# Optimization experiments

Hardware: AMD Instinct MI355X
Metric: run time of the kernel (lower is better)

## Reference

```python
import jax, jax.numpy as jnp
import numpy as np

H = 128
P, L, C = 1024, 1024, 128
NT, NH, NA, NB, NPA, NPE = 64, 32, 64, 64, 32, 32


def _ln(x, g, b):
    m = jnp.mean(x, -1, keepdims=True)
    v = jnp.var(x, -1, keepdims=True)
    return (x - m) * jax.lax.rsqrt(v + 1e-5) * g + b


def _lrl(x, W, b, g, be):
    # Linear -> ReLU -> LayerNorm (the Sequential block used everywhere)
    return _ln(jax.nn.relu(x @ W.T + b), g, be)


def _combine(middle, margin, rel):
    # margin-middle-margin combine: aggregate related margin geos on both sides
    # rel: (M, G) 0/1 float; middle (M,h); margin (G,h)
    agg = rel @ margin                      # (M, h)
    comb = agg + middle + agg
    mask = (jnp.sum(rel, -1) >= 2.0).astype(middle.dtype)  # need two margins
    return comb, mask


def _score(sym, geo, mask, W1, b1, g, be, W2, b2):
    # pairwise sym x geo -> Linear/ReLU/LN -> Linear(h,1), masked, sigmoid
    pair = sym[:, None, :] + geo[None, :, :]          # (N, R, h)
    hdn = _lrl(pair, W1, b1, g, be)
    logits = hdn @ W2 + b2                            # (N, R)
    return jax.nn.sigmoid(jnp.where(mask[None, :] > 0, logits, -1e9))


def setup_inputs() -> dict:
    key = jax.random.key(0)
    ks = jax.random.split(key, 16)
    s = 0.02
    inp = {
        'points': jax.random.normal(ks[0], (P, H), jnp.float32),
        'lines': jax.random.normal(ks[1], (L, H), jnp.float32),
        'circles': jax.random.normal(ks[2], (C, H), jnp.float32),
        'text_symbols': jax.random.normal(ks[3], (NT, H), jnp.float32),
        'head_symbols': jax.random.normal(ks[4], (NH, H), jnp.float32),
        'angle_symbols': jax.random.normal(ks[5], (NA, H), jnp.float32),
        'bar_symbols': jax.random.normal(ks[6], (NB, H), jnp.float32),
        'parallel_symbols': jax.random.normal(ks[7], (NPA, H), jnp.float32),
        'perpendicular_symbols': jax.random.normal(ks[8], (NPE, H), jnp.float32),
        'rel_W': jax.random.normal(ks[9], (3, H, H), jnp.float32) * s,
        'rel_b': jnp.zeros((3, H), jnp.float32),
        'rel_g': jnp.ones((3, H), jnp.float32),
        'rel_be': jnp.zeros((3, H), jnp.float32),
        'gm_W': jax.random.normal(ks[10], (2, H, H), jnp.float32) * s,
        'gm_b': jnp.zeros((2, H), jnp.float32),
        'gm_g': jnp.ones((2, H), jnp.float32),
        'gm_be': jnp.zeros((2, H), jnp.float32),
        'sc_W1': jax.random.normal(ks[11], (6, H, H), jnp.float32) * s,
        'sc_b1': jnp.zeros((6, H), jnp.float32),
        'sc_g': jnp.ones((6, H), jnp.float32),
        'sc_be': jnp.zeros((6, H), jnp.float32),
        'sc_W2': jax.random.normal(ks[12], (6, H), jnp.float32) * s,
        'sc_b2': jnp.zeros((6,), jnp.float32),
        'pl_rels': jax.random.randint(ks[13], (P, L), 0, 2, jnp.int32),
        'pc_rels': jax.random.randint(ks[14], (P, C), 0, 2, jnp.int32),
    }
    return inp


def reference(points, lines, circles, text_symbols, head_symbols,
              angle_symbols, bar_symbols, parallel_symbols, perpendicular_symbols,
              rel_W, rel_b, rel_g, rel_be, gm_W, gm_b, gm_g, gm_be,
              sc_W1, sc_b1, sc_g, sc_be, sc_W2, sc_b2, pl_rels, pc_rels):
    pl = pl_rels.astype(points.dtype)            # (P, L)
    pc = pc_rels.astype(points.dtype)            # (P, C)

    # LPL: middle=points, margin=lines, rel=pl_rels
    lpl_c, lpl_m = _combine(points, lines, pl)
    LPL = _lrl(lpl_c, rel_W[0], rel_b[0], rel_g[0], rel_be[0])   # (P, h)
    # PLP: middle=lines, margin=points, rel=pl_rels.T
    plp_c, plp_m = _combine(lines, points, pl.T)
    PLP = _lrl(plp_c, rel_W[1], rel_b[1], rel_g[1], rel_be[1])   # (L, h)
    # PCP: middle=circles, margin=points, rel=pc_rels.T
    pcp_c, pcp_m = _combine(circles, points, pc.T)
    PCP = _lrl(pcp_c, rel_W[2], rel_b[2], rel_g[2], rel_be[2])   # (C, h)

    ones = lambda n: jnp.ones((n,), points.dtype)

    def gm(x):
        x = _lrl(x, gm_W[0], gm_b[0], gm_g[0], gm_be[0])
        return _lrl(x, gm_W[1], gm_b[1], gm_g[1], gm_be[1])

    # text symbols vs (P, L, LPL, PLP, PCP, head)
    geo_t = jnp.concatenate([points, lines, LPL, PLP, PCP, head_symbols], 0)
    mask_t = jnp.concatenate([ones(P), ones(L), lpl_m, plp_m, pcp_m, ones(NH)], 0)
    text = _score(text_symbols, gm(geo_t), mask_t,
                  sc_W1[0], sc_b1[0], sc_g[0], sc_be[0], sc_W2[0], sc_b2[0])

    # head symbols vs (P, LPL, PLP, PCP)
    geo_h = jnp.concatenate([points, LPL, PLP, PCP], 0)
    mask_h = jnp.concatenate([ones(P), lpl_m, plp_m, pcp_m], 0)
    head = _score(head_symbols, gm(geo_h), mask_h,
                  sc_W1[1], sc_b1[1], sc_g[1], sc_be[1], sc_W2[1], sc_b2[1])

    angle = _score(angle_symbols, LPL, lpl_m,
                   sc_W1[2], sc_b1[2], sc_g[2], sc_be[2], sc_W2[2], sc_b2[2])
    bar = _score(bar_symbols, PLP, plp_m,
                 sc_W1[3], sc_b1[3], sc_g[3], sc_be[3], sc_W2[3], sc_b2[3])
    para = _score(parallel_symbols, lines, ones(L),
                  sc_W1[4], sc_b1[4], sc_g[4], sc_be[4], sc_W2[4], sc_b2[4])
    perp = _score(perpendicular_symbols, LPL, lpl_m,
                  sc_W1[5], sc_b1[5], sc_g[5], sc_be[5], sc_W2[5], sc_b2[5])

    return jnp.concatenate([text.ravel(), head.ravel(), angle.ravel(),
                            bar.ravel(), para.ravel(), perp.ravel()])
```

## Files before the change

kernel.cpp:

```cpp
#include <hip/hip_runtime.h>

#define HH 128

constexpr int OFF_AGGPL = 0;
constexpr int OFF_AGGLP = OFF_AGGPL + 1024*HH;
constexpr int OFF_AGGCP = OFF_AGGLP + 1024*HH;
constexpr int OFF_MLPL  = OFF_AGGCP + 128*HH;
constexpr int OFF_MPLP  = OFF_MLPL + 1024;
constexpr int OFF_MPCP  = OFF_MPLP + 1024;
constexpr int OFF_LPL   = OFF_MPCP + 128;
constexpr int OFF_PLP   = OFF_LPL + 1024*HH;
constexpr int OFF_PCP   = OFF_PLP + 1024*HH;
constexpr int OFF_G1    = OFF_PCP + 128*HH;
constexpr int OFF_GT    = OFF_G1 + 4256*HH;
constexpr int OFF_BTEXT = OFF_GT + 4256*HH;
constexpr int OFF_BHEAD = OFF_BTEXT + 4256*HH;
constexpr int OFF_BANG  = OFF_BHEAD + 3200*HH;
constexpr int OFF_BBAR  = OFF_BANG + 1024*HH;
constexpr int OFF_BPARA = OFF_BBAR + 1024*HH;
constexpr int OFF_BPERP = OFF_BPARA + 1024*HH;
constexpr int OFF_A     = OFF_BPERP + 1024*HH;
constexpr int WS_FLOATS = OFF_A + 288*HH;

__global__ __launch_bounds__(512) void k_agg(
    const int* __restrict__ pl, const int* __restrict__ pc,
    const float* __restrict__ points, const float* __restrict__ lines,
    float* __restrict__ ws)
{
    __shared__ __attribute__((aligned(16))) float smem[16384];
    float (*rel)[1024] = (float(*)[1024])smem;
    float* red = smem;
    const int t = threadIdx.x;
    const int b = blockIdx.x;
    const int hq  = t & 31;
    const int grp = t >> 5;

    const float* V; float* OUT; float* MASK; int base;
    if (b < 128) {
        base = b*8; V = lines; OUT = ws + OFF_AGGPL; MASK = ws + OFF_MLPL;
        const int4* pl4 = (const int4*)pl;
        #pragma unroll
        for (int i = 0; i < 4; ++i) {
            int idx = i*512 + t; int r = idx >> 8, lq = idx & 255;
            int4 v = pl4[(base + r)*256 + lq];
            float4 f; f.x=(float)v.x; f.y=(float)v.y; f.z=(float)v.z; f.w=(float)v.w;
            *(float4*)&rel[r][lq*4] = f;
        }
    } else if (b < 256) {
        base = (b-128)*8; V = points; OUT = ws + OFF_AGGLP; MASK = ws + OFF_MPLP;
        #pragma unroll
        for (int i = 0; i < 16; ++i) {
            int idx = i*512 + t; int c = idx & 7, k = idx >> 3;
            rel[c][k] = (float)pl[k*1024 + base + c];
        }
    } else {
        base = (b-256)*8; V = points; OUT = ws + OFF_AGGCP; MASK = ws + OFF_MPCP;
        #pragma unroll
        for (int i = 0; i < 16; ++i) {
            int idx = i*512 + t; int c = idx & 7, k = idx >> 3;
            rel[c][k] = (float)pc[k*128 + base + c];
        }
    }
    __syncthreads();
    {
        int r = t >> 6, lane = t & 63;
        float s = 0.f;
        #pragma unroll
        for (int i = 0; i < 16; ++i) s += rel[r][lane*16 + i];
        #pragma unroll
        for (int off = 32; off; off >>= 1) s += __shfl_xor(s, off, 64);
        if (lane == 0) MASK[base + r] = (s >= 2.0f) ? 1.0f : 0.0f;
    }

    float4 acc[8];
    #pragma unroll
    for (int r = 0; r < 8; ++r) acc[r] = {0.f, 0.f, 0.f, 0.f};
    const float4* V4 = (const float4*)V;
    const int l0 = grp * 64;
    #pragma unroll 4
    for (int l = l0; l < l0 + 64; l += 4) {
        float4 v0 = V4[(l+0)*32 + hq];
        float4 v1 = V4[(l+1)*32 + hq];
        float4 v2 = V4[(l+2)*32 + hq];
        float4 v3 = V4[(l+3)*32 + hq];
        #pragma unroll
        for (int r = 0; r < 8; ++r) {
            float4 rv = *(const float4*)&rel[r][l];
            acc[r].x += rv.x*v0.x + rv.y*v1.x + rv.z*v2.x + rv.w*v3.x;
            acc[r].y += rv.x*v0.y + rv.y*v1.y + rv.z*v2.y + rv.w*v3.y;
            acc[r].z += rv.x*v0.z + rv.y*v1.z + rv.z*v2.z + rv.w*v3.z;
            acc[r].w += rv.x*v0.w + rv.y*v1.w + rv.z*v2.w + rv.w*v3.w;
        }
    }
    __syncthreads();
    #pragma unroll
    for (int r = 0; r < 8; ++r)
        *(float4*)&red[(grp*8 + r)*128 + hq*4] = acc[r];
    __syncthreads();
    #pragma unroll
    for (int o = t; o < 1024; o += 512) {
        int r = o >> 7, c = o & 127;
        float s = 0.f;
        #pragma unroll
        for (int g2 = 0; g2 < 16; ++g2) s += red[g2*1024 + r*128 + c];
        OUT[(base + r)*HH + c] = s;
    }
}

__global__ __launch_bounds__(256) void k_lrl(
    int mode, float* __restrict__ ws,
    const float* __restrict__ points, const float* __restrict__ lines,
    const float* __restrict__ circles, const float* __restrict__ text_s,
    const float* __restrict__ head_s, const float* __restrict__ angle_s,
    const float* __restrict__ bar_s, const float* __restrict__ para_s,
    const float* __restrict__ perp_s,
    const float* __restrict__ rel_W, const float* __restrict__ rel_b,
    const float* __restrict__ rel_g, const float* __restrict__ rel_be,
    const float* __restrict__ gm_W, const float* __restrict__ gm_b,
    const float* __restrict__ gm_g, const float* __restrict__ gm_be,
    const float* __restrict__ sc_W1, const float* __restrict__ sc_b1)
{
    __shared__ __attribute__((aligned(16))) float Xs[32][132];
    __shared__ __attribute__((aligned(16))) float Ws[64][132];
    const int t = threadIdx.x;
    const int row0 = blockIdx.x * 32;

    const float* W = nullptr; const float* bias = nullptr;
    const float* gv = nullptr; const float* bev = nullptr;
    const float* xsrc = nullptr; const float* asrc = nullptr; const float* msrc = nullptr;
    float* outp = nullptr;
    bool do_ln = false;

    if (mode == 0) {
        do_ln = true;
        if (row0 < 1024) {
            asrc = ws + OFF_AGGPL + row0*HH; msrc = points + row0*HH;
            W = rel_W;          bias = rel_b;       gv = rel_g;       bev = rel_be;
            outp = ws + OFF_LPL + row0*HH;
        } else if (row0 < 2048) {
            int r = row0 - 1024;
            asrc = ws + OFF_AGGLP + r*HH; msrc = lines + r*HH;
            W = rel_W + 16384;  bias = rel_b + 128; gv = rel_g + 128; bev = rel_be + 128;
            outp = ws + OFF_PLP + r*HH;
        } else {
            int r = row0 - 2048;
            asrc = ws + OFF_AGGCP + r*HH; msrc = circles + r*HH;
            W = rel_W + 32768;  bias = rel_b + 256; gv = rel_g + 256; bev = rel_be + 256;
            outp = ws + OFF_PCP + r*HH;
        }
    } else if (mode == 1) {
        do_ln = true; W = gm_W; bias = gm_b; gv = gm_g; bev = gm_be;
        outp = ws + OFF_G1 + row0*HH;
        if      (row0 < 1024) xsrc = points + row0*HH;
        else if (row0 < 2048) xsrc = lines + (row0-1024)*HH;
        else if (row0 < 3072) xsrc = ws + OFF_LPL + (row0-2048)*HH;
        else if (row0 < 4096) xsrc = ws + OFF_PLP + (row0-3072)*HH;
        else if (row0 < 4224) xsrc = ws + OFF_PCP + (row0-4096)*HH;
        else                  xsrc = head_s + (row0-4224)*HH;
    } else if (mode == 2) {
        do_ln = true; W = gm_W + 16384; bias = gm_b + 128; gv = gm_g + 128; bev = gm_be + 128;
        xsrc = ws + OFF_G1 + row0*HH;
        outp = ws + OFF_GT + row0*HH;
    } else {
        do_ln = false;
        if (row0 < 4256) {
            xsrc = ws + OFF_GT + row0*HH; W = sc_W1; outp = ws + OFF_BTEXT + row0*HH;
        } else if (row0 < 7456) {
            int i0 = row0 - 4256;
            W = sc_W1 + 16384; outp = ws + OFF_BHEAD + i0*HH;
            int gtrow;
            if      (i0 < 1024) gtrow = i0;
            else if (i0 < 2048) gtrow = 2048 + (i0 - 1024);
            else if (i0 < 3072) gtrow = 3072 + (i0 - 2048);
            else                gtrow = 4096 + (i0 - 3072);
            xsrc = ws + OFF_GT + gtrow*HH;
        } else if (row0 < 8480) {
            int i0 = row0 - 7456;
            xsrc = ws + OFF_LPL + i0*HH; W = sc_W1 + 2*16384; outp = ws + OFF_BANG + i0*HH;
        } else if (row0 < 9504) {
            int i0 = row0 - 8480;
            xsrc = ws + OFF_PLP + i0*HH; W = sc_W1 + 3*16384; outp = ws + OFF_BBAR + i0*HH;
        } else if (row0 < 10528) {
            int i0 = row0 - 9504;
            xsrc = lines + i0*HH;        W = sc_W1 + 4*16384; outp = ws + OFF_BPARA + i0*HH;
        } else if (row0 < 11552) {
            int i0 = row0 - 10528;
            xsrc = ws + OFF_LPL + i0*HH; W = sc_W1 + 5*16384; outp = ws + OFF_BPERP + i0*HH;
        } else {
            int i0 = row0 - 11552;
            outp = ws + OFF_A + i0*HH;
            int k; const float* s;
            if      (i0 < 64)  { k=0; s = text_s  + i0*HH; }
            else if (i0 < 96)  { k=1; s = head_s  + (i0-64)*HH; }
            else if (i0 < 160) { k=2; s = angle_s + (i0-96)*HH; }
            else if (i0 < 224) { k=3; s = bar_s   + (i0-160)*HH; }
            else if (i0 < 256) { k=4; s = para_s  + (i0-224)*HH; }
            else               { k=5; s = perp_s  + (i0-256)*HH; }
            xsrc = s; W = sc_W1 + k*16384; bias = sc_b1 + k*128;
        }
    }

    if (asrc != nullptr) {
        #pragma unroll
        for (int i = 0; i < 4; ++i) {
            int idx = i*256 + t; int r = idx >> 5, hq = idx & 31;
            float4 a = *(const float4*)&asrc[r*HH + hq*4];
            float4 m = *(const float4*)&msrc[r*HH + hq*4];
            float4 v; v.x = 2.f*a.x+m.x; v.y = 2.f*a.y+m.y; v.z = 2.f*a.z+m.z; v.w = 2.f*a.w+m.w;
            *(float4*)&Xs[r][hq*4] = v;
        }
    } else {
        #pragma unroll
        for (int i = 0; i < 4; ++i) {
            int idx = i*256 + t; int r = idx >> 5, hq = idx & 31;
            *(float4*)&Xs[r][hq*4] = *(const float4*)&xsrc[r*HH + hq*4];
        }
    }

    const int jq = t & 31;
    const int rq = t >> 5;
    float acc[4][4] = {};
    for (int p = 0; p < 2; ++p) {
        __syncthreads();
        #pragma unroll
        for (int i = 0; i < 8; ++i) {
            int idx = i*256 + t; int j = idx >> 4, hq = idx & 15;
            float4 v = *(const float4*)&W[j*HH + p*64 + hq*4];
            Ws[hq*4+0][j] = v.x; Ws[hq*4+1][j] = v.y; Ws[hq*4+2][j] = v.z; Ws[hq*4+3][j] = v.w;
        }
        __syncthreads();
        #pragma unroll
        for (int hh = 0; hh < 64; hh += 4) {
            const int h = p*64 + hh;
            float4 x0 = *(const float4*)&Xs[rq*4+0][h];
            float4 x1 = *(const float4*)&Xs[rq*4+1][h];
            float4 x2 = *(const float4*)&Xs[rq*4+2][h];
            float4 x3 = *(const float4*)&Xs[rq*4+3][h];
            float4 w0 = *(const float4*)&Ws[hh+0][jq*4];
            float4 w1 = *(const float4*)&Ws[hh+1][jq*4];
            float4 w2 = *(const float4*)&Ws[hh+2][jq*4];
            float4 w3 = *(const float4*)&Ws[hh+3][jq*4];
            #define ROWUPD(ri, xv) \
                acc[ri][0] += xv.x*w0.x + xv.y*w1.x + xv.z*w2.x + xv.w*w3.x; \
                acc[ri][1] += xv.x*w0.y + xv.y*w1.y + xv.z*w2.y + xv.w*w3.y; \
                acc[ri][2] += xv.x*w0.z + xv.y*w1.z + xv.z*w2.z + xv.w*w3.z; \
                acc[ri][3] += xv.x*w0.w + xv.y*w1.w + xv.z*w2.w + xv.w*w3.w;
            ROWUPD(0, x0) ROWUPD(1, x1) ROWUPD(2, x2) ROWUPD(3, x3)
            #undef ROWUPD
        }
    }

    float4 bv = {0.f,0.f,0.f,0.f};
    if (bias != nullptr) bv = *(const float4*)&bias[jq*4];
    if (do_ln) {
        float4 gg = *(const float4*)&gv[jq*4];
        float4 bb = *(const float4*)&bev[jq*4];
        #pragma unroll
        for (int ri = 0; ri < 4; ++ri) {
            float y0 = fmaxf(acc[ri][0] + bv.x, 0.f);
            float y1 = fmaxf(acc[ri][1] + bv.y, 0.f);
            float y2 = fmaxf(acc[ri][2] + bv.z, 0.f);
            float y3 = fmaxf(acc[ri][3] + bv.w, 0.f);
            float s1 = y0+y1+y2+y3;
            float s2 = y0*y0+y1*y1+y2*y2+y3*y3;
            #pragma unroll
            for (int off = 16; off; off >>= 1) {
                s1 += __shfl_xor(s1, off, 32);
                s2 += __shfl_xor(s2, off, 32);
            }
            float m   = s1 * (1.0f/128.0f);
            float var = s2 * (1.0f/128.0f) - m*m;
            float sc  = rsqrtf(var + 1e-5f);
            float4 o;
            o.x = (y0 - m)*sc*gg.x + bb.x;
            o.y = (y1 - m)*sc*gg.y + bb.y;
            o.z = (y2 - m)*sc*gg.z + bb.z;
            o.w = (y3 - m)*sc*gg.w + bb.w;
            *(float4*)&outp[(rq*4+ri)*HH + jq*4] = o;
        }
    } else {
        #pragma unroll
        for (int ri = 0; ri < 4; ++ri) {
            float4 o;
            o.x = acc[ri][0] + bv.x; o.y = acc[ri][1] + bv.y;
            o.z = acc[ri][2] + bv.z; o.w = acc[ri][3] + bv.w;
            *(float4*)&outp[(rq*4+ri)*HH + jq*4] = o;
        }
    }
}

__global__ __launch_bounds__(256) void k_score(
    const float* __restrict__ ws,
    const float* __restrict__ sc_g, const float* __restrict__ sc_be,
    const float* __restrict__ sc_W2, const float* __restrict__ sc_b2,
    float* __restrict__ out)
{
    __shared__ __attribute__((aligned(16))) float As[16][132];
    __shared__ __attribute__((aligned(16))) float Bs[16][132];
    __shared__ __attribute__((aligned(16))) float gw2s[128];
    __shared__ float msk[16];
    __shared__ float red2[4];
    const int t = threadIdx.x, b = blockIdx.x;
    int k, tn, tr, Rk, Abase, outbase;
    const float* Bk;
    if (b < 1064)      { k=0; int lc=b;      tn=lc/266; tr=lc%266; Rk=4256; Abase=0;   outbase=0;      Bk = ws+OFF_BTEXT; }
    else if (b < 1464) { k=1; int lc=b-1064; tn=lc/200; tr=lc%200; Rk=3200; Abase=64;  outbase=272384; Bk = ws+OFF_BHEAD; }
    else if (b < 1720) { k=2; int lc=b-1464; tn=lc>>6;  tr=lc&63;  Rk=1024; Abase=96;  outbase=374784; Bk = ws+OFF_BANG; }
    else if (b < 1976) { k=3; int lc=b-1720; tn=lc>>6;  tr=lc&63;  Rk=1024; Abase=160; outbase=440320; Bk = ws+OFF_BBAR; }
    else if (b < 2104) { k=4; int lc=b-1976; tn=lc>>6;  tr=lc&63;  Rk=1024; Abase=224; outbase=505856; Bk = ws+OFF_BPARA; }
    else               { k=5; int lc=b-2104; tn=lc>>6;  tr=lc&63;  Rk=1024; Abase=256; outbase=538624; Bk = ws+OFF_BPERP; }

    if (t < 128) {
        float g = sc_g[k*128+t], w2 = sc_W2[k*128+t], be = sc_be[k*128+t];
        float gw = g*w2, bw = be*w2;
        gw2s[t] = gw;
        #pragma unroll
        for (int off = 32; off; off >>= 1) {
            gw += __shfl_xor(gw, off, 64);
            bw += __shfl_xor(bw, off, 64);
        }
        if ((t & 63) == 0) { red2[(t>>6)*2+0] = gw; red2[(t>>6)*2+1] = bw; }
    }
    const float* Ap = ws + OFF_A + (Abase + tn*16)*HH;
    const float* Bp = Bk + tr*16*HH;
    #pragma unroll
    for (int i = 0; i < 2; ++i) {
        int idx = i*256 + t; int r = idx >> 5, hq = idx & 31;
        *(float4*)&As[r][hq*4] = *(const float4*)&Ap[r*HH + hq*4];
        *(float4*)&Bs[r][hq*4] = *(const float4*)&Bp[r*HH + hq*4];
    }
    if (t < 16) {
        int r = tr*16 + t;
        float mv = 1.0f;
        const float* mL = ws + OFF_MLPL;
        const float* mP = ws + OFF_MPLP;
        const float* mC = ws + OFF_MPCP;
        if (k == 0) {
            if      (r >= 2048 && r < 3072) mv = mL[r-2048];
            else if (r >= 3072 && r < 4096) mv = mP[r-3072];
            else if (r >= 4096 && r < 4224) mv = mC[r-4096];
        } else if (k == 1) {
            if      (r >= 1024 && r < 2048) mv = mL[r-1024];
            else if (r >= 2048 && r < 3072) mv = mP[r-2048];
            else if (r >= 3072)             mv = mC[r-3072];
        } else if (k == 2 || k == 5) mv = mL[r];
        else if (k == 3)             mv = mP[r];
        msk[t] = mv;
    }
    __syncthreads();
    const float sgw2 = red2[0] + red2[2];
    const float cb   = red2[1] + red2[3] + sc_b2[k];
    const int ni = t >> 4, ri = t & 15;
    float s1 = 0.f, s2 = 0.f, sw = 0.f;
    #pragma unroll
    for (int h = 0; h < 128; h += 4) {
        float4 av = *(const float4*)&As[ni][h];
        float4 bv = *(const float4*)&Bs[ri][h];
        float4 wv = *(const float4*)&gw2s[h];
        float y;
        y = fmaxf(av.x + bv.x, 0.f); s1 += y; s2 += y*y; sw += y*wv.x;
        y = fmaxf(av.y + bv.y, 0.f); s1 += y; s2 += y*y; sw += y*wv.y;
        y = fmaxf(av.z + bv.z, 0.f); s1 += y; s2 += y*y; sw += y*wv.z;
        y = fmaxf(av.w + bv.w, 0.f); s1 += y; s2 += y*y; sw += y*wv.w;
    }
    float m   = s1 * (1.0f/128.0f);
    float var = s2 * (1.0f/128.0f) - m*m;
    float logit = (sw - m*sgw2) * rsqrtf(var + 1e-5f) + cb;
    float o = (msk[ri] > 0.f) ? (1.0f/(1.0f + __expf(-logit))) : 0.0f;
    out[outbase + (tn*16+ni)*Rk + tr*16 + ri] = o;
}

extern "C" void kernel_launch(void* const* d_in, const int* in_sizes, int n_in,
                              void* d_out, int out_size, void* d_ws, size_t ws_size,
                              hipStream_t stream)
{
    const float* points  = (const float*)d_in[0];
    const float* lines   = (const float*)d_in[1];
    const float* circles = (const float*)d_in[2];
    const float* text_s  = (const float*)d_in[3];
    const float* head_s  = (const float*)d_in[4];
    const float* angle_s = (const float*)d_in[5];
    const float* bar_s   = (const float*)d_in[6];
    const float* para_s  = (const float*)d_in[7];
    const float* perp_s  = (const float*)d_in[8];
    const float* rel_W   = (const float*)d_in[9];
    const float* rel_b   = (const float*)d_in[10];
    const float* rel_g   = (const float*)d_in[11];
    const float* rel_be  = (const float*)d_in[12];
    const float* gm_W    = (const float*)d_in[13];
    const float* gm_b    = (const float*)d_in[14];
    const float* gm_g    = (const float*)d_in[15];
    const float* gm_be   = (const float*)d_in[16];
    const float* sc_W1   = (const float*)d_in[17];
    const float* sc_b1   = (const float*)d_in[18];
    const float* sc_g    = (const float*)d_in[19];
    const float* sc_be   = (const float*)d_in[20];
    const float* sc_W2   = (const float*)d_in[21];
    const float* sc_b2   = (const float*)d_in[22];
    const int*   pl      = (const int*)d_in[23];
    const int*   pc      = (const int*)d_in[24];
    float* ws  = (float*)d_ws;
    float* out = (float*)d_out;
    if (ws_size < (size_t)WS_FLOATS * sizeof(float)) return;

    hipLaunchKernelGGL(k_agg, dim3(272), dim3(512), 0, stream, pl, pc, points, lines, ws);
    #define LRL_ARGS ws, points, lines, circles, text_s, head_s, angle_s, bar_s, para_s, perp_s, \
        rel_W, rel_b, rel_g, rel_be, gm_W, gm_b, gm_g, gm_be, sc_W1, sc_b1
    hipLaunchKernelGGL(k_lrl, dim3(68),  dim3(256), 0, stream, 0, LRL_ARGS);
    hipLaunchKernelGGL(k_lrl, dim3(133), dim3(256), 0, stream, 1, LRL_ARGS);
    hipLaunchKernelGGL(k_lrl, dim3(133), dim3(256), 0, stream, 2, LRL_ARGS);
    hipLaunchKernelGGL(k_lrl, dim3(370), dim3(256), 0, stream, 3, LRL_ARGS);
    #undef LRL_ARGS
    hipLaunchKernelGGL(k_score, dim3(2232), dim3(256), 0, stream, ws, sc_g, sc_be, sc_W2, sc_b2, out);
}
```

Measured before the change: 194.7 us.

## Enlarge score tiles to 32x32 with 2x2 register blocking; widen LRL blocks

The pairwise score kernel now handles 32x32 symbol-geo tiles per block instead of 16x16. Each thread computes a 2x2 group of pairs, so every shared-memory float4 load is reused across two pairs, and the grid shrinks fourfold. The LRL GEMM kernel moves to 512 threads, each computing 2 rows instead of 4, which raises parallelism per block but lowers register reuse. The padded shared rows (140) are meant to cut bank conflicts, at the cost of fewer blocks overall and more registers per thread.

```diff
diff --git a/kernel.cpp b/kernel.cpp
--- a/kernel.cpp
+++ b/kernel.cpp
@@ -107,7 +107,7 @@
     }
 }
 
-__global__ __launch_bounds__(256) void k_lrl(
+__global__ __launch_bounds__(512) void k_lrl(
     int mode, float* __restrict__ ws,
     const float* __restrict__ points, const float* __restrict__ lines,
     const float* __restrict__ circles, const float* __restrict__ text_s,
@@ -202,8 +202,8 @@
 
     if (asrc != nullptr) {
         #pragma unroll
-        for (int i = 0; i < 4; ++i) {
-            int idx = i*256 + t; int r = idx >> 5, hq = idx & 31;
+        for (int i = 0; i < 2; ++i) {
+            int idx = i*512 + t; int r = idx >> 5, hq = idx & 31;
             float4 a = *(const float4*)&asrc[r*HH + hq*4];
             float4 m = *(const float4*)&msrc[r*HH + hq*4];
             float4 v; v.x = 2.f*a.x+m.x; v.y = 2.f*a.y+m.y; v.z = 2.f*a.z+m.z; v.w = 2.f*a.w+m.w;
@@ -211,20 +211,20 @@
         }
     } else {
         #pragma unroll
-        for (int i = 0; i < 4; ++i) {
-            int idx = i*256 + t; int r = idx >> 5, hq = idx & 31;
+        for (int i = 0; i < 2; ++i) {
+            int idx = i*512 + t; int r = idx >> 5, hq = idx & 31;
             *(float4*)&Xs[r][hq*4] = *(const float4*)&xsrc[r*HH + hq*4];
         }
     }
 
     const int jq = t & 31;
     const int rq = t >> 5;
-    float acc[4][4] = {};
+    float acc[2][4] = {};
     for (int p = 0; p < 2; ++p) {
         __syncthreads();
         #pragma unroll
-        for (int i = 0; i < 8; ++i) {
-            int idx = i*256 + t; int j = idx >> 4, hq = idx & 15;
+        for (int i = 0; i < 4; ++i) {
+            int idx = i*512 + t; int j = idx >> 4, hq = idx & 15;
             float4 v = *(const float4*)&W[j*HH + p*64 + hq*4];
             Ws[hq*4+0][j] = v.x; Ws[hq*4+1][j] = v.y; Ws[hq*4+2][j] = v.z; Ws[hq*4+3][j] = v.w;
         }
@@ -232,10 +232,8 @@
         #pragma unroll
         for (int hh = 0; hh < 64; hh += 4) {
             const int h = p*64 + hh;
-            float4 x0 = *(const float4*)&Xs[rq*4+0][h];
-            float4 x1 = *(const float4*)&Xs[rq*4+1][h];
-            float4 x2 = *(const float4*)&Xs[rq*4+2][h];
-            float4 x3 = *(const float4*)&Xs[rq*4+3][h];
+            float4 x0 = *(const float4*)&Xs[rq*2+0][h];
+            float4 x1 = *(const float4*)&Xs[rq*2+1][h];
             float4 w0 = *(const float4*)&Ws[hh+0][jq*4];
             float4 w1 = *(const float4*)&Ws[hh+1][jq*4];
             float4 w2 = *(const float4*)&Ws[hh+2][jq*4];
@@ -245,7 +243,7 @@
                 acc[ri][1] += xv.x*w0.y + xv.y*w1.y + xv.z*w2.y + xv.w*w3.y; \
                 acc[ri][2] += xv.x*w0.z + xv.y*w1.z + xv.z*w2.z + xv.w*w3.z; \
                 acc[ri][3] += xv.x*w0.w + xv.y*w1.w + xv.z*w2.w + xv.w*w3.w;
-            ROWUPD(0, x0) ROWUPD(1, x1) ROWUPD(2, x2) ROWUPD(3, x3)
+            ROWUPD(0, x0) ROWUPD(1, x1)
             #undef ROWUPD
         }
     }
@@ -256,7 +254,7 @@
         float4 gg = *(const float4*)&gv[jq*4];
         float4 bb = *(const float4*)&bev[jq*4];
         #pragma unroll
-        for (int ri = 0; ri < 4; ++ri) {
+        for (int ri = 0; ri < 2; ++ri) {
             float y0 = fmaxf(acc[ri][0] + bv.x, 0.f);
             float y1 = fmaxf(acc[ri][1] + bv.y, 0.f);
             float y2 = fmaxf(acc[ri][2] + bv.z, 0.f);
@@ -276,15 +274,15 @@
             o.y = (y1 - m)*sc*gg.y + bb.y;
             o.z = (y2 - m)*sc*gg.z + bb.z;
             o.w = (y3 - m)*sc*gg.w + bb.w;
-            *(float4*)&outp[(rq*4+ri)*HH + jq*4] = o;
+            *(float4*)&outp[(rq*2+ri)*HH + jq*4] = o;
         }
     } else {
         #pragma unroll
-        for (int ri = 0; ri < 4; ++ri) {
+        for (int ri = 0; ri < 2; ++ri) {
             float4 o;
             o.x = acc[ri][0] + bv.x; o.y = acc[ri][1] + bv.y;
             o.z = acc[ri][2] + bv.z; o.w = acc[ri][3] + bv.w;
-            *(float4*)&outp[(rq*4+ri)*HH + jq*4] = o;
+            *(float4*)&outp[(rq*2+ri)*HH + jq*4] = o;
         }
     }
 }
@@ -295,20 +293,20 @@
     const float* __restrict__ sc_W2, const float* __restrict__ sc_b2,
     float* __restrict__ out)
 {
-    __shared__ __attribute__((aligned(16))) float As[16][132];
-    __shared__ __attribute__((aligned(16))) float Bs[16][132];
+    __shared__ __attribute__((aligned(16))) float As[32][140];
+    __shared__ __attribute__((aligned(16))) float Bs[32][140];
     __shared__ __attribute__((aligned(16))) float gw2s[128];
-    __shared__ float msk[16];
+    __shared__ float msk[32];
     __shared__ float red2[4];
     const int t = threadIdx.x, b = blockIdx.x;
     int k, tn, tr, Rk, Abase, outbase;
     const float* Bk;
-    if (b < 1064)      { k=0; int lc=b;      tn=lc/266; tr=lc%266; Rk=4256; Abase=0;   outbase=0;      Bk = ws+OFF_BTEXT; }
-    else if (b < 1464) { k=1; int lc=b-1064; tn=lc/200; tr=lc%200; Rk=3200; Abase=64;  outbase=272384; Bk = ws+OFF_BHEAD; }
-    else if (b < 1720) { k=2; int lc=b-1464; tn=lc>>6;  tr=lc&63;  Rk=1024; Abase=96;  outbase=374784; Bk = ws+OFF_BANG; }
-    else if (b < 1976) { k=3; int lc=b-1720; tn=lc>>6;  tr=lc&63;  Rk=1024; Abase=160; outbase=440320; Bk = ws+OFF_BBAR; }
-    else if (b < 2104) { k=4; int lc=b-1976; tn=lc>>6;  tr=lc&63;  Rk=1024; Abase=224; outbase=505856; Bk = ws+OFF_BPARA; }
-    else               { k=5; int lc=b-2104; tn=lc>>6;  tr=lc&63;  Rk=1024; Abase=256; outbase=538624; Bk = ws+OFF_BPERP; }
+    if (b < 266)      { k=0; int lc=b;     tn=lc/133; tr=lc%133; Rk=4256; Abase=0;   outbase=0;      Bk = ws+OFF_BTEXT; }
+    else if (b < 366) { k=1; int lc=b-266; tn=0;      tr=lc;     Rk=3200; Abase=64;  outbase=272384; Bk = ws+OFF_BHEAD; }
+    else if (b < 430) { k=2; int lc=b-366; tn=lc>>5;  tr=lc&31;  Rk=1024; Abase=96;  outbase=374784; Bk = ws+OFF_BANG; }
+    else if (b < 494) { k=3; int lc=b-430; tn=lc>>5;  tr=lc&31;  Rk=1024; Abase=160; outbase=440320; Bk = ws+OFF_BBAR; }
+    else if (b < 526) { k=4; int lc=b-494; tn=0;      tr=lc;     Rk=1024; Abase=224; outbase=505856; Bk = ws+OFF_BPARA; }
+    else              { k=5; int lc=b-526; tn=0;      tr=lc;     Rk=1024; Abase=256; outbase=538624; Bk = ws+OFF_BPERP; }
 
     if (t < 128) {
         float g = sc_g[k*128+t], w2 = sc_W2[k*128+t], be = sc_be[k*128+t];
@@ -321,16 +319,16 @@
         }
         if ((t & 63) == 0) { red2[(t>>6)*2+0] = gw; red2[(t>>6)*2+1] = bw; }
     }
-    const float* Ap = ws + OFF_A + (Abase + tn*16)*HH;
-    const float* Bp = Bk + tr*16*HH;
-    #pragma unroll
-    for (int i = 0; i < 2; ++i) {
+    const float* Ap = ws + OFF_A + (Abase + tn*32)*HH;
+    const float* Bp = Bk + tr*32*HH;
+    #pragma unroll
+    for (int i = 0; i < 4; ++i) {
         int idx = i*256 + t; int r = idx >> 5, hq = idx & 31;
         *(float4*)&As[r][hq*4] = *(const float4*)&Ap[r*HH + hq*4];
         *(float4*)&Bs[r][hq*4] = *(const float4*)&Bp[r*HH + hq*4];
     }
-    if (t < 16) {
-        int r = tr*16 + t;
+    if (t < 32) {
+        int r = tr*32 + t;
         float mv = 1.0f;
         const float* mL = ws + OFF_MLPL;
         const float* mP = ws + OFF_MPLP;
@@ -350,24 +348,35 @@
     __syncthreads();
     const float sgw2 = red2[0] + red2[2];
     const float cb   = red2[1] + red2[3] + sc_b2[k];
-    const int ni = t >> 4, ri = t & 15;
-    float s1 = 0.f, s2 = 0.f, sw = 0.f;
+    const int n2 = t >> 4;
+    const int r2 = t & 15;
+    float s1[4] = {}, s2[4] = {}, sw[4] = {};
     #pragma unroll
     for (int h = 0; h < 128; h += 4) {
-        float4 av = *(const float4*)&As[ni][h];
-        float4 bv = *(const float4*)&Bs[ri][h];
+        float4 a0 = *(const float4*)&As[n2*2+0][h];
+        float4 a1 = *(const float4*)&As[n2*2+1][h];
+        float4 b0 = *(const float4*)&Bs[r2*2+0][h];
+        float4 b1 = *(const float4*)&Bs[r2*2+1][h];
         float4 wv = *(const float4*)&gw2s[h];
         float y;
-        y = fmaxf(av.x + bv.x, 0.f); s1 += y; s2 += y*y; sw += y*wv.x;
-        y = fmaxf(av.y + bv.y, 0.f); s1 += y; s2 += y*y; sw += y*wv.y;
-        y = fmaxf(av.z + bv.z, 0.f); s1 += y; s2 += y*y; sw += y*wv.z;
-        y = fmaxf(av.w + bv.w, 0.f); s1 += y; s2 += y*y; sw += y*wv.w;
-    }
-    float m   = s1 * (1.0f/128.0f);
-    float var = s2 * (1.0f/128.0f) - m*m;
-    float logit = (sw - m*sgw2) * rsqrtf(var + 1e-5f) + cb;
-    float o = (msk[ri] > 0.f) ? (1.0f/(1.0f + __expf(-logit))) : 0.0f;
-    out[outbase + (tn*16+ni)*Rk + tr*16 + ri] = o;
+        #define PUPD(pi, av, bv2) \
+            y = fmaxf(av.x + bv2.x, 0.f); s1[pi] += y; s2[pi] += y*y; sw[pi] += y*wv.x; \
+            y = fmaxf(av.y + bv2.y, 0.f); s1[pi] += y; s2[pi] += y*y; sw[pi] += y*wv.y; \
+            y = fmaxf(av.z + bv2.z, 0.f); s1[pi] += y; s2[pi] += y*y; sw[pi] += y*wv.z; \
+            y = fmaxf(av.w + bv2.w, 0.f); s1[pi] += y; s2[pi] += y*y; sw[pi] += y*wv.w;
+        PUPD(0, a0, b0) PUPD(1, a0, b1) PUPD(2, a1, b0) PUPD(3, a1, b1)
+        #undef PUPD
+    }
+    #pragma unroll
+    for (int pi = 0; pi < 4; ++pi) {
+        int ni = n2*2 + (pi >> 1);
+        int ri = r2*2 + (pi & 1);
+        float m   = s1[pi] * (1.0f/128.0f);
+        float var = s2[pi] * (1.0f/128.0f) - m*m;
+        float logit = (sw[pi] - m*sgw2) * rsqrtf(var + 1e-5f) + cb;
+        float o = (msk[ri] > 0.f) ? (1.0f/(1.0f + __expf(-logit))) : 0.0f;
+        out[outbase + (tn*32+ni)*Rk + tr*32 + ri] = o;
+    }
 }
 
 extern "C" void kernel_launch(void* const* d_in, const int* in_sizes, int n_in,
@@ -406,10 +415,10 @@
     hipLaunchKernelGGL(k_agg, dim3(272), dim3(512), 0, stream, pl, pc, points, lines, ws);
     #define LRL_ARGS ws, points, lines, circles, text_s, head_s, angle_s, bar_s, para_s, perp_s, \
         rel_W, rel_b, rel_g, rel_be, gm_W, gm_b, gm_g, gm_be, sc_W1, sc_b1
-    hipLaunchKernelGGL(k_lrl, dim3(68),  dim3(256), 0, stream, 0, LRL_ARGS);
-    hipLaunchKernelGGL(k_lrl, dim3(133), dim3(256), 0, stream, 1, LRL_ARGS);
-    hipLaunchKernelGGL(k_lrl, dim3(133), dim3(256), 0, stream, 2, LRL_ARGS);
-    hipLaunchKernelGGL(k_lrl, dim3(370), dim3(256), 0, stream, 3, LRL_ARGS);
+    hipLaunchKernelGGL(k_lrl, dim3(68),  dim3(512), 0, stream, 0, LRL_ARGS);
+    hipLaunchKernelGGL(k_lrl, dim3(133), dim3(512), 0, stream, 1, LRL_ARGS);
+    hipLaunchKernelGGL(k_lrl, dim3(133), dim3(512), 0, stream, 2, LRL_ARGS);
+    hipLaunchKernelGGL(k_lrl, dim3(370), dim3(512), 0, stream, 3, LRL_ARGS);
     #undef LRL_ARGS
-    hipLaunchKernelGGL(k_score, dim3(2232), dim3(256), 0, stream, ws, sc_g, sc_be, sc_W2, sc_b2, out);
+    hipLaunchKernelGGL(k_score, dim3(558), dim3(256), 0, stream, ws, sc_g, sc_be, sc_W2, sc_b2, out);
 }
```

Measured after the change: 327.4 us. +68.2%, slower.
